# Optimization experiments

Measured on AMD Instinct MI355X. Metric: run time of the kernel, lower is better.

Reference implementation:

```python
import jax, jax.numpy as jnp
import numpy as np

B, D, H = 8192, 256, 512


def setup_inputs() -> dict:
    key = jax.random.key(0)
    ks = jax.random.split(key, 25)
    inp = {
        "x": jax.random.normal(ks[0], (B, D), jnp.float32),
        "h_t": jax.random.normal(ks[1], (B, H), jnp.float32),
        "h_s": jax.random.normal(ks[2], (B, H), jnp.float32),
        "c_t": jax.random.normal(ks[3], (B, H), jnp.float32),
        "c_s": jax.random.normal(ks[4], (B, H), jnp.float32),
    }
    names = ["Ui", "Wti", "Wsi", "bi", "Us", "Wts", "Wss", "bs",
             "Ut", "Wtt", "Wst", "bt", "Uo", "Wto", "Wso", "bo",
             "Uc", "Wtc", "Wsc", "bc"]
    shapes = {"U": (D, H), "W": (H, H), "b": (H,)}
    scale = 0.02  # keep activations in a sane range
    for i, n in enumerate(names):
        s = shapes["U"] if n[0] == "U" else (shapes["b"] if n[0] == "b" else shapes["W"])
        inp[n] = jax.random.normal(ks[5 + i], s, jnp.float32) * scale
    return inp


def reference(x, h_t, h_s, c_t, c_s,
              Ui, Wti, Wsi, bi, Us, Wts, Wss, bs,
              Ut, Wtt, Wst, bt, Uo, Wto, Wso, bo,
              Uc, Wtc, Wsc, bc):
    # Fuse the 15 small GEMMs into 3 concatenated GEMMs: [B,D]@[D,5H] etc.
    U = jnp.concatenate([Ui, Us, Ut, Uo, Uc], axis=1)      # [D, 5H]
    Wt = jnp.concatenate([Wti, Wts, Wtt, Wto, Wtc], axis=1)  # [H, 5H]
    Ws = jnp.concatenate([Wsi, Wss, Wst, Wso, Wsc], axis=1)  # [H, 5H]
    b = jnp.concatenate([bi, bs, bt, bo, bc])                # [5H]
    gates = x @ U + h_t @ Wt + h_s @ Ws + b                  # [B, 5H]
    g_i, g_fs, g_ft, g_o, g_c = jnp.split(gates, 5, axis=1)
    i_n = jax.nn.sigmoid(g_i)
    f_s_n = jax.nn.sigmoid(g_fs)
    f_t_n = jax.nn.sigmoid(g_ft)
    o_n = jax.nn.sigmoid(g_o)
    c_n = jnp.tanh(g_c)
    c_h = i_n * c_n + f_t_n * c_t + f_s_n * c_s
    h = o_n * jnp.tanh(c_h)
    return (h, c_h)
```

## Files before the change

### kernel.cpp

```cpp
#include <hip/hip_runtime.h>
#include <hip/hip_bf16.h>
#include <cstdint>
#include <cstddef>

#define B_  8192
#define D_  256
#define H_  512
#define K_  1280
#define N_  2560
#define NT_ 320
#define BM_ 256
#define BK_ 64

typedef short short8  __attribute__((ext_vector_type(8)));
typedef float f32x4   __attribute__((ext_vector_type(4)));
typedef float f32x16  __attribute__((ext_vector_type(16)));

__device__ __forceinline__ float sigf(float x)     { return 1.f / (1.f + __expf(-x)); }
__device__ __forceinline__ float tanhfast(float x) { return 1.f - 2.f / (__expf(2.f * x) + 1.f); }

struct WPtrs {
    const float* U[5];
    const float* Wt[5];
    const float* Ws[5];
};

__global__ void prep_a_kernel(const float* __restrict__ x, const float* __restrict__ ht,
                              const float* __restrict__ hs, __hip_bfloat16* __restrict__ A) {
    int t = blockIdx.x * 256 + threadIdx.x;
    int idx8 = t * 8;
    int b = idx8 / K_;
    int k = idx8 - b * K_;
    const float* src;
    if (k < D_)            src = x  + (size_t)b * D_ + k;
    else if (k < D_ + H_)  src = ht + (size_t)b * H_ + (k - D_);
    else                   src = hs + (size_t)b * H_ + (k - D_ - H_);
    f32x4 v0 = *(const f32x4*)(src);
    f32x4 v1 = *(const f32x4*)(src + 4);
    union { short8 s; __hip_bfloat16 h[8]; } o;
    o.h[0] = __float2bfloat16(v0[0]); o.h[1] = __float2bfloat16(v0[1]);
    o.h[2] = __float2bfloat16(v0[2]); o.h[3] = __float2bfloat16(v0[3]);
    o.h[4] = __float2bfloat16(v1[0]); o.h[5] = __float2bfloat16(v1[1]);
    o.h[6] = __float2bfloat16(v1[2]); o.h[7] = __float2bfloat16(v1[3]);
    *(short8*)(A + idx8) = o.s;
}

__global__ void prep_w_kernel(WPtrs p, __hip_bfloat16* __restrict__ WT) {
    __shared__ __hip_bfloat16 tile[64][66];
    int bid2 = blockIdx.x;
    int hblk = bid2 & 7;
    int kblk = (bid2 >> 3) % 20;
    int g    = bid2 / 160;
    int k0 = kblk * 64;
    int h0 = hblk * 64;
    const float* src; int kl0;
    if (k0 < 256)      { src = p.U[g];  kl0 = k0; }
    else if (k0 < 768) { src = p.Wt[g]; kl0 = k0 - 256; }
    else               { src = p.Ws[g]; kl0 = k0 - 768; }
    int tid = threadIdx.x;
    int tk = tid >> 6;
    int th = tid & 63;
    for (int r = 0; r < 16; ++r) {
        int kl = r * 4 + tk;
        tile[kl][th] = __float2bfloat16(src[(size_t)(kl0 + kl) * H_ + h0 + th]);
    }
    __syncthreads();
    for (int r = 0; r < 16; ++r) {
        int hl = r * 4 + tk;
        int h  = h0 + hl;
        int np = (h >> 5) * 160 + g * 32 + (h & 31);
        WT[(size_t)np * K_ + k0 + th] = tile[th][hl];
    }
}

#define GLD16(gp, lp)                                                              \
    __builtin_amdgcn_global_load_lds(                                              \
        (const __attribute__((address_space(1))) unsigned int*)(gp),               \
        (__attribute__((address_space(3))) unsigned int*)(lp), 16, 0, 0)

__global__ __launch_bounds__(512, 2) void gemm_fused_kernel(
    const __hip_bfloat16* __restrict__ A, const __hip_bfloat16* __restrict__ WT,
    const float* __restrict__ ct, const float* __restrict__ cs,
    const float* __restrict__ bi, const float* __restrict__ bfs,
    const float* __restrict__ bft, const float* __restrict__ bo,
    const float* __restrict__ bc, float* __restrict__ out) {
    __shared__ alignas(16) unsigned short sA[2][BM_ * BK_];
    __shared__ alignas(16) unsigned short sB[2][NT_ * BK_];

    int tid = threadIdx.x;
    int n0 = blockIdx.x * NT_;
    int m0 = blockIdx.y * BM_;
    int wid  = tid >> 6, lane = tid & 63;
    int wm   = wid >> 1;
    int wn   = wid & 1;
    int half = lane >> 5, l31 = lane & 31;

    int hg = blockIdx.x * 2 + wn;
    int h  = hg * 32 + l31;
    float Bi = bi[h], Bfs = bfs[h], Bft = bft[h], Bo = bo[h], Bc = bc[h];

    f32x16 acc[2][5];
#pragma unroll
    for (int i = 0; i < 2; ++i)
#pragma unroll
        for (int j = 0; j < 5; ++j)
            acc[i][j] = (f32x16)(0.f);

    int srow = tid >> 3;
    int cSw  = (tid & 7) ^ (srow & 7);
    const __hip_bfloat16* aSrcB = A  + (size_t)(m0 + srow) * K_ + cSw * 8;
    const __hip_bfloat16* bSrcB = WT + (size_t)(n0 + srow) * K_ + cSw * 8;
    int t8 = tid * 8;

#define STAGE(bufsel, koff)                                                      \
    do {                                                                         \
        _Pragma("unroll")                                                        \
        for (int r_ = 0; r_ < 4; ++r_)                                           \
            GLD16(aSrcB + (size_t)r_ * 64 * K_ + (koff), sA[bufsel] + r_ * 4096 + t8); \
        _Pragma("unroll")                                                        \
        for (int r_ = 0; r_ < 5; ++r_)                                           \
            GLD16(bSrcB + (size_t)r_ * 64 * K_ + (koff), sB[bufsel] + r_ * 4096 + t8); \
    } while (0)

    int arow64[2], brow64[5];
#pragma unroll
    for (int i = 0; i < 2; ++i) arow64[i] = (wm * 64 + i * 32 + l31) * 64;
#pragma unroll
    for (int j = 0; j < 5; ++j) brow64[j] = (wn * 160 + j * 32 + l31) * 64;
    int xr = l31 & 7;
    int pk[4];
#pragma unroll
    for (int ks = 0; ks < 4; ++ks) pk[ks] = ((ks * 2 + half) ^ xr) * 8;

    STAGE(0, 0);
    __syncthreads();

    const int nt = K_ / BK_;
#pragma unroll 2
    for (int t = 0; t < nt; ++t) {
        int cur = t & 1;
        if (t + 1 < nt) STAGE(cur ^ 1, (t + 1) * BK_);
        const unsigned short* sAc = sA[cur];
        const unsigned short* sBc = sB[cur];
#pragma unroll
        for (int ks = 0; ks < 4; ++ks) {
            short8 a[2], b[5];
            int po = pk[ks];
#pragma unroll
            for (int i = 0; i < 2; ++i)
                a[i] = *(const short8*)(sAc + arow64[i] + po);
#pragma unroll
            for (int j = 0; j < 5; ++j)
                b[j] = *(const short8*)(sBc + brow64[j] + po);
            __builtin_amdgcn_s_setprio(1);
#pragma unroll
            for (int j = 0; j < 5; ++j)
#pragma unroll
                for (int i = 0; i < 2; ++i)
                    acc[i][j] = __builtin_amdgcn_mfma_f32_32x32x16_bf16(a[i], b[j], acc[i][j], 0, 0, 0);
            __builtin_amdgcn_s_setprio(0);
        }
        __syncthreads();
    }
#undef STAGE

#pragma unroll
    for (int i = 0; i < 2; ++i) {
        int rbase = m0 + wm * 64 + i * 32 + 4 * half;
#pragma unroll
        for (int r = 0; r < 16; ++r) {
            int row = rbase + (r & 3) + 8 * (r >> 2);
            size_t idx = (size_t)row * H_ + h;
            float i_n  = sigf(acc[i][0][r] + Bi);
            float fs_n = sigf(acc[i][1][r] + Bfs);
            float ft_n = sigf(acc[i][2][r] + Bft);
            float o_n  = sigf(acc[i][3][r] + Bo);
            float c_n  = tanhfast(acc[i][4][r] + Bc);
            float ch   = i_n * c_n + ft_n * ct[idx] + fs_n * cs[idx];
            out[idx] = o_n * tanhfast(ch);
            out[(size_t)B_ * H_ + idx] = ch;
        }
    }
}

struct AllW {
    const float* U[5];
    const float* Wt[5];
    const float* Ws[5];
    const float* bias[5];
};

__global__ __launch_bounds__(512) void fallback_kernel(const float* __restrict__ x,
                                                       const float* __restrict__ ht,
                                                       const float* __restrict__ hs,
                                                       const float* __restrict__ ct,
                                                       const float* __restrict__ cs,
                                                       AllW w, float* __restrict__ out) {
    __shared__ float arow[K_];
    int b = blockIdx.x;
    int h = threadIdx.x;
    for (int k = h; k < K_; k += 512) {
        float v;
        if (k < D_)           v = x[b * D_ + k];
        else if (k < D_ + H_) v = ht[b * H_ + k - D_];
        else                  v = hs[b * H_ + k - D_ - H_];
        arow[k] = v;
    }
    __syncthreads();
    float g[5];
    for (int gi = 0; gi < 5; ++gi) {
        float s = w.bias[gi][h];
        const float* U = w.U[gi];
        for (int k = 0; k < D_; ++k) s += arow[k] * U[(size_t)k * H_ + h];
        const float* Wt = w.Wt[gi];
        for (int k = 0; k < H_; ++k) s += arow[D_ + k] * Wt[(size_t)k * H_ + h];
        const float* Ws = w.Ws[gi];
        for (int k = 0; k < H_; ++k) s += arow[D_ + H_ + k] * Ws[(size_t)k * H_ + h];
        g[gi] = s;
    }
    int idx = b * H_ + h;
    float i_n = sigf(g[0]), fs_n = sigf(g[1]), ft_n = sigf(g[2]), o_n = sigf(g[3]);
    float c_n = tanhfast(g[4]);
    float ch  = i_n * c_n + ft_n * ct[idx] + fs_n * cs[idx];
    out[idx] = o_n * tanhfast(ch);
    out[(size_t)B_ * H_ + idx] = ch;
}

extern "C" void kernel_launch(void* const* d_in, const int* in_sizes, int n_in,
                              void* d_out, int out_size, void* d_ws, size_t ws_size,
                              hipStream_t stream) {
    const float* x  = (const float*)d_in[0];
    const float* ht = (const float*)d_in[1];
    const float* hs = (const float*)d_in[2];
    const float* ct = (const float*)d_in[3];
    const float* cs = (const float*)d_in[4];

    WPtrs wp;
    AllW  aw;
    const float* bias[5];
    for (int g = 0; g < 5; ++g) {
        wp.U[g]  = (const float*)d_in[5 + g * 4 + 0];
        wp.Wt[g] = (const float*)d_in[5 + g * 4 + 1];
        wp.Ws[g] = (const float*)d_in[5 + g * 4 + 2];
        bias[g]  = (const float*)d_in[5 + g * 4 + 3];
        aw.U[g] = wp.U[g]; aw.Wt[g] = wp.Wt[g]; aw.Ws[g] = wp.Ws[g]; aw.bias[g] = bias[g];
    }
    float* out = (float*)d_out;

    size_t szA = (size_t)B_ * K_ * 2;
    size_t szW = (size_t)N_ * K_ * 2;

    if (ws_size >= szA + szW) {
        __hip_bfloat16* Abf = (__hip_bfloat16*)d_ws;
        __hip_bfloat16* WT  = (__hip_bfloat16*)((char*)d_ws + szA);

        prep_a_kernel<<<5120, 256, 0, stream>>>(x, ht, hs, Abf);
        prep_w_kernel<<<800, 256, 0, stream>>>(wp, WT);
        gemm_fused_kernel<<<dim3(N_ / NT_, B_ / BM_), 512, 0, stream>>>(
            Abf, WT, ct, cs, bias[0], bias[1], bias[2], bias[3], bias[4], out);
    } else {
        fallback_kernel<<<B_, 512, 0, stream>>>(x, ht, hs, ct, cs, aw, out);
    }
}
```

Before: 234.5 us.

## Halve GEMM block to 256 threads with 4x5 MFMA tiles per wave

The fused GEMM now runs 256 threads (4 waves) per block instead of 512. Each wave computes a 128x160 output tile (4x5 MFMA 32x32 accumulators) instead of 64x160, which raises register-level reuse of the B fragments. The grid is transposed so blockIdx.x walks M, and the LDS swizzle is changed to a 4-way XOR on (row>>1). The price is 320 accumulator registers per lane and single-block occupancy, which could cause spills or poor latency hiding. Global-to-LDS staging now issues twice as many loads per thread.

```diff
diff --git a/kernel.cpp b/kernel.cpp
--- a/kernel.cpp
+++ b/kernel.cpp
@@ -78,7 +78,7 @@
         (const __attribute__((address_space(1))) unsigned int*)(gp),               \
         (__attribute__((address_space(3))) unsigned int*)(lp), 16, 0, 0)
 
-__global__ __launch_bounds__(512, 2) void gemm_fused_kernel(
+__global__ __launch_bounds__(256, 1) void gemm_fused_kernel(
     const __hip_bfloat16* __restrict__ A, const __hip_bfloat16* __restrict__ WT,
     const float* __restrict__ ct, const float* __restrict__ cs,
     const float* __restrict__ bi, const float* __restrict__ bfs,
@@ -88,75 +88,76 @@
     __shared__ alignas(16) unsigned short sB[2][NT_ * BK_];
 
     int tid = threadIdx.x;
-    int n0 = blockIdx.x * NT_;
-    int m0 = blockIdx.y * BM_;
+    int m0 = blockIdx.x * BM_;
+    int n0 = blockIdx.y * NT_;
     int wid  = tid >> 6, lane = tid & 63;
     int wm   = wid >> 1;
     int wn   = wid & 1;
     int half = lane >> 5, l31 = lane & 31;
 
-    int hg = blockIdx.x * 2 + wn;
+    int hg = blockIdx.y * 2 + wn;
     int h  = hg * 32 + l31;
     float Bi = bi[h], Bfs = bfs[h], Bft = bft[h], Bo = bo[h], Bc = bc[h];
 
-    f32x16 acc[2][5];
-#pragma unroll
-    for (int i = 0; i < 2; ++i)
+    f32x16 acc[4][5];
+#pragma unroll
+    for (int i = 0; i < 4; ++i)
 #pragma unroll
         for (int j = 0; j < 5; ++j)
             acc[i][j] = (f32x16)(0.f);
 
-    int srow = tid >> 3;
-    int cSw  = (tid & 7) ^ (srow & 7);
-    const __hip_bfloat16* aSrcB = A  + (size_t)(m0 + srow) * K_ + cSw * 8;
-    const __hip_bfloat16* bSrcB = WT + (size_t)(n0 + srow) * K_ + cSw * 8;
+    int r0  = tid >> 3;
+    int kcS = ((tid & 7) ^ ((r0 >> 1) & 3)) * 8;
+    const __hip_bfloat16* aBase = A  + (size_t)(m0 + r0) * K_ + kcS;
+    const __hip_bfloat16* bBase = WT + (size_t)(n0 + r0) * K_ + kcS;
     int t8 = tid * 8;
 
-#define STAGE(bufsel, koff)                                                      \
-    do {                                                                         \
-        _Pragma("unroll")                                                        \
-        for (int r_ = 0; r_ < 4; ++r_)                                           \
-            GLD16(aSrcB + (size_t)r_ * 64 * K_ + (koff), sA[bufsel] + r_ * 4096 + t8); \
-        _Pragma("unroll")                                                        \
-        for (int r_ = 0; r_ < 5; ++r_)                                           \
-            GLD16(bSrcB + (size_t)r_ * 64 * K_ + (koff), sB[bufsel] + r_ * 4096 + t8); \
+#define STAGE(bufsel, koff)                                                       \
+    do {                                                                          \
+        _Pragma("unroll")                                                         \
+        for (int i_ = 0; i_ < 8; ++i_)                                            \
+            GLD16(aBase + (size_t)i_ * 32 * K_ + (koff), sA[bufsel] + i_ * 2048 + t8); \
+        _Pragma("unroll")                                                         \
+        for (int i_ = 0; i_ < 10; ++i_)                                           \
+            GLD16(bBase + (size_t)i_ * 32 * K_ + (koff), sB[bufsel] + i_ * 2048 + t8); \
     } while (0)
 
-    int arow64[2], brow64[5];
-#pragma unroll
-    for (int i = 0; i < 2; ++i) arow64[i] = (wm * 64 + i * 32 + l31) * 64;
-#pragma unroll
-    for (int j = 0; j < 5; ++j) brow64[j] = (wn * 160 + j * 32 + l31) * 64;
-    int xr = l31 & 7;
-    int pk[4];
-#pragma unroll
-    for (int ks = 0; ks < 4; ++ks) pk[ks] = ((ks * 2 + half) ^ xr) * 8;
+    int arow[4], brow[5], aswz[4], bswz[5];
+#pragma unroll
+    for (int i = 0; i < 4; ++i) {
+        arow[i] = (wm * 128 + i * 32 + l31);
+        aswz[i] = (arow[i] >> 1) & 3;
+    }
+#pragma unroll
+    for (int j = 0; j < 5; ++j) {
+        brow[j] = (wn * 160 + j * 32 + l31);
+        bswz[j] = (brow[j] >> 1) & 3;
+    }
 
     STAGE(0, 0);
     __syncthreads();
 
     const int nt = K_ / BK_;
-#pragma unroll 2
     for (int t = 0; t < nt; ++t) {
         int cur = t & 1;
-        if (t + 1 < nt) STAGE(cur ^ 1, (t + 1) * BK_);
+        if (t + 1 < nt) STAGE(cur ^ 1, (size_t)(t + 1) * BK_);
         const unsigned short* sAc = sA[cur];
         const unsigned short* sBc = sB[cur];
 #pragma unroll
         for (int ks = 0; ks < 4; ++ks) {
-            short8 a[2], b[5];
-            int po = pk[ks];
-#pragma unroll
-            for (int i = 0; i < 2; ++i)
-                a[i] = *(const short8*)(sAc + arow64[i] + po);
+            short8 a[4], b[5];
+            int g = ks * 2 + half;
+#pragma unroll
+            for (int i = 0; i < 4; ++i)
+                a[i] = *(const short8*)(sAc + arow[i] * 64 + (g ^ aswz[i]) * 8);
 #pragma unroll
             for (int j = 0; j < 5; ++j)
-                b[j] = *(const short8*)(sBc + brow64[j] + po);
+                b[j] = *(const short8*)(sBc + brow[j] * 64 + (g ^ bswz[j]) * 8);
             __builtin_amdgcn_s_setprio(1);
 #pragma unroll
             for (int j = 0; j < 5; ++j)
 #pragma unroll
-                for (int i = 0; i < 2; ++i)
+                for (int i = 0; i < 4; ++i)
                     acc[i][j] = __builtin_amdgcn_mfma_f32_32x32x16_bf16(a[i], b[j], acc[i][j], 0, 0, 0);
             __builtin_amdgcn_s_setprio(0);
         }
@@ -165,8 +166,8 @@
 #undef STAGE
 
 #pragma unroll
-    for (int i = 0; i < 2; ++i) {
-        int rbase = m0 + wm * 64 + i * 32 + 4 * half;
+    for (int i = 0; i < 4; ++i) {
+        int rbase = m0 + wm * 128 + i * 32 + 4 * half;
 #pragma unroll
         for (int r = 0; r < 16; ++r) {
             int row = rbase + (r & 3) + 8 * (r >> 2);
@@ -256,7 +257,7 @@
 
         prep_a_kernel<<<5120, 256, 0, stream>>>(x, ht, hs, Abf);
         prep_w_kernel<<<800, 256, 0, stream>>>(wp, WT);
-        gemm_fused_kernel<<<dim3(N_ / NT_, B_ / BM_), 512, 0, stream>>>(
+        gemm_fused_kernel<<<dim3(B_ / BM_, N_ / NT_), 256, 0, stream>>>(
             Abf, WT, ct, cs, bias[0], bias[1], bias[2], bias[3], bias[4], out);
     } else {
         fallback_kernel<<<B_, 512, 0, stream>>>(x, ht, hs, ct, cs, aw, out);
```

Result: slower. 339.9 us (+44.9%).

## Interleave global-to-LDS prefetch across k-substeps with explicit barriers and waitcnts

Applied to the files above, without the earlier changes.

Restructures the main GEMM loop so the next tile's global-to-LDS loads are split across the four k-substeps (A first, then B in two chunks) instead of issued all at once. Each substep reads its LDS fragments, then uses explicit s_barrier and lgkmcnt/vmcnt waits before and after the MFMAs, similar to a ping-pong schedule. The aim is to spread memory traffic and overlap it better with MFMA work. The cost is eight barriers per k-tile instead of one, which may add synchronisation stalls.

```diff
diff --git a/kernel.cpp b/kernel.cpp
--- a/kernel.cpp
+++ b/kernel.cpp
@@ -94,6 +94,7 @@
     int wm   = wid >> 1;
     int wn   = wid & 1;
     int half = lane >> 5, l31 = lane & 31;
+    int xr   = l31 & 7;
 
     int hg = blockIdx.x * 2 + wn;
     int h  = hg * 32 + l31;
@@ -107,62 +108,106 @@
             acc[i][j] = (f32x16)(0.f);
 
     int srow = tid >> 3;
-    int cSw  = (tid & 7) ^ (srow & 7);
-    const __hip_bfloat16* aSrcB = A  + (size_t)(m0 + srow) * K_ + cSw * 8;
-    const __hip_bfloat16* bSrcB = WT + (size_t)(n0 + srow) * K_ + cSw * 8;
+    int kcS  = ((tid & 7) ^ (srow & 7)) * 8;
+    const __hip_bfloat16* aBase = A  + (size_t)(m0 + srow) * K_ + kcS;
+    const __hip_bfloat16* bBase = WT + (size_t)(n0 + srow) * K_ + kcS;
     int t8 = tid * 8;
 
-#define STAGE(bufsel, koff)                                                      \
-    do {                                                                         \
-        _Pragma("unroll")                                                        \
-        for (int r_ = 0; r_ < 4; ++r_)                                           \
-            GLD16(aSrcB + (size_t)r_ * 64 * K_ + (koff), sA[bufsel] + r_ * 4096 + t8); \
-        _Pragma("unroll")                                                        \
-        for (int r_ = 0; r_ < 5; ++r_)                                           \
-            GLD16(bSrcB + (size_t)r_ * 64 * K_ + (koff), sB[bufsel] + r_ * 4096 + t8); \
+#define STG_A(dst, koff)                                                        \
+    do {                                                                        \
+        _Pragma("unroll")                                                       \
+        for (int r_ = 0; r_ < 4; ++r_)                                          \
+            GLD16(aBase + (size_t)r_ * 64 * K_ + (koff), (dst) + r_ * 4096 + t8); \
     } while (0)
+#define STG_B(dst, koff, rlo, rhi)                                              \
+    do {                                                                        \
+        _Pragma("unroll")                                                       \
+        for (int r_ = (rlo); r_ < (rhi); ++r_)                                  \
+            GLD16(bBase + (size_t)r_ * 64 * K_ + (koff), (dst) + r_ * 4096 + t8); \
+    } while (0)
 
     int arow64[2], brow64[5];
 #pragma unroll
     for (int i = 0; i < 2; ++i) arow64[i] = (wm * 64 + i * 32 + l31) * 64;
 #pragma unroll
     for (int j = 0; j < 5; ++j) brow64[j] = (wn * 160 + j * 32 + l31) * 64;
-    int xr = l31 & 7;
-    int pk[4];
-#pragma unroll
-    for (int ks = 0; ks < 4; ++ks) pk[ks] = ((ks * 2 + half) ^ xr) * 8;
-
-    STAGE(0, 0);
-    __syncthreads();
+
+#define READS(ks_)                                                              \
+    int po_ = (((ks_) * 2 + half) ^ xr) * 8;                                    \
+    short8 a0 = *(const short8*)(sAc + arow64[0] + po_);                        \
+    short8 a1 = *(const short8*)(sAc + arow64[1] + po_);                        \
+    short8 b0 = *(const short8*)(sBc + brow64[0] + po_);                        \
+    short8 b1 = *(const short8*)(sBc + brow64[1] + po_);                        \
+    short8 b2 = *(const short8*)(sBc + brow64[2] + po_);                        \
+    short8 b3 = *(const short8*)(sBc + brow64[3] + po_);                        \
+    short8 b4 = *(const short8*)(sBc + brow64[4] + po_)
+
+#define MFMAS()                                                                 \
+    __builtin_amdgcn_s_setprio(1);                                              \
+    acc[0][0] = __builtin_amdgcn_mfma_f32_32x32x16_bf16(a0, b0, acc[0][0], 0, 0, 0); \
+    acc[1][0] = __builtin_amdgcn_mfma_f32_32x32x16_bf16(a1, b0, acc[1][0], 0, 0, 0); \
+    acc[0][1] = __builtin_amdgcn_mfma_f32_32x32x16_bf16(a0, b1, acc[0][1], 0, 0, 0); \
+    acc[1][1] = __builtin_amdgcn_mfma_f32_32x32x16_bf16(a1, b1, acc[1][1], 0, 0, 0); \
+    acc[0][2] = __builtin_amdgcn_mfma_f32_32x32x16_bf16(a0, b2, acc[0][2], 0, 0, 0); \
+    acc[1][2] = __builtin_amdgcn_mfma_f32_32x32x16_bf16(a1, b2, acc[1][2], 0, 0, 0); \
+    acc[0][3] = __builtin_amdgcn_mfma_f32_32x32x16_bf16(a0, b3, acc[0][3], 0, 0, 0); \
+    acc[1][3] = __builtin_amdgcn_mfma_f32_32x32x16_bf16(a1, b3, acc[1][3], 0, 0, 0); \
+    acc[0][4] = __builtin_amdgcn_mfma_f32_32x32x16_bf16(a0, b4, acc[0][4], 0, 0, 0); \
+    acc[1][4] = __builtin_amdgcn_mfma_f32_32x32x16_bf16(a1, b4, acc[1][4], 0, 0, 0); \
+    __builtin_amdgcn_s_setprio(0)
+
+#define BAR()   __builtin_amdgcn_s_barrier()
+#define LGKM0() asm volatile("s_waitcnt lgkmcnt(0)" ::: "memory")
+#define VM0()   asm volatile("s_waitcnt vmcnt(0)" ::: "memory")
+
+    STG_A(sA[0], 0);
+    STG_B(sB[0], 0, 0, 5);
+    VM0();
+    BAR();
 
     const int nt = K_ / BK_;
 #pragma unroll 2
     for (int t = 0; t < nt; ++t) {
-        int cur = t & 1;
-        if (t + 1 < nt) STAGE(cur ^ 1, (t + 1) * BK_);
-        const unsigned short* sAc = sA[cur];
-        const unsigned short* sBc = sB[cur];
-#pragma unroll
-        for (int ks = 0; ks < 4; ++ks) {
-            short8 a[2], b[5];
-            int po = pk[ks];
-#pragma unroll
-            for (int i = 0; i < 2; ++i)
-                a[i] = *(const short8*)(sAc + arow64[i] + po);
-#pragma unroll
-            for (int j = 0; j < 5; ++j)
-                b[j] = *(const short8*)(sBc + brow64[j] + po);
-            __builtin_amdgcn_s_setprio(1);
-#pragma unroll
-            for (int j = 0; j < 5; ++j)
-#pragma unroll
-                for (int i = 0; i < 2; ++i)
-                    acc[i][j] = __builtin_amdgcn_mfma_f32_32x32x16_bf16(a[i], b[j], acc[i][j], 0, 0, 0);
-            __builtin_amdgcn_s_setprio(0);
-        }
-        __syncthreads();
-    }
-#undef STAGE
+        const unsigned short* sAc = sA[t & 1];
+        const unsigned short* sBc = sB[t & 1];
+        unsigned short* sAn = sA[(t & 1) ^ 1];
+        unsigned short* sBn = sB[(t & 1) ^ 1];
+        const bool pf = (t + 1 < nt);
+        const int ko = (t + 1) * BK_;
+
+        {
+            if (pf) STG_A(sAn, ko);
+            READS(0);
+            BAR(); LGKM0();
+            MFMAS();
+            BAR();
+        }
+        {
+            if (pf) STG_B(sBn, ko, 0, 3);
+            READS(1);
+            BAR(); LGKM0();
+            MFMAS();
+            BAR();
+        }
+        {
+            if (pf) STG_B(sBn, ko, 3, 5);
+            READS(2);
+            BAR(); LGKM0();
+            MFMAS();
+            BAR();
+        }
+        {
+            READS(3);
+            BAR(); LGKM0();
+            MFMAS();
+            VM0();
+            BAR();
+        }
+    }
+#undef STG_A
+#undef STG_B
+#undef READS
+#undef MFMAS
 
 #pragma unroll
     for (int i = 0; i < 2; ++i) {
```

Result: slower. 241.3 us (+2.9%).

## Fuse fp32-to-bf16 activation conversion into GEMM A-tile loading

Applied to the files above, without the earlier changes.

Drops the separate prep kernel that turned x, h_t and h_s into a bf16 concatenated A matrix. The GEMM now loads fp32 activations straight into registers, converts them and writes the swizzled bf16 tile into LDS, interleaved with the MFMA k-steps. This removes one kernel launch and the write and re-read of the bf16 A buffer. In exchange each GEMM block reads fp32 A (twice the bytes) once per N-tile column (8 column blocks), and the A loads become synchronous register loads instead of async global-to-LDS copies, which may add latency and register pressure.

```diff
diff --git a/kernel.cpp b/kernel.cpp
--- a/kernel.cpp
+++ b/kernel.cpp
@@ -24,26 +24,6 @@
     const float* Wt[5];
     const float* Ws[5];
 };
-
-__global__ void prep_a_kernel(const float* __restrict__ x, const float* __restrict__ ht,
-                              const float* __restrict__ hs, __hip_bfloat16* __restrict__ A) {
-    int t = blockIdx.x * 256 + threadIdx.x;
-    int idx8 = t * 8;
-    int b = idx8 / K_;
-    int k = idx8 - b * K_;
-    const float* src;
-    if (k < D_)            src = x  + (size_t)b * D_ + k;
-    else if (k < D_ + H_)  src = ht + (size_t)b * H_ + (k - D_);
-    else                   src = hs + (size_t)b * H_ + (k - D_ - H_);
-    f32x4 v0 = *(const f32x4*)(src);
-    f32x4 v1 = *(const f32x4*)(src + 4);
-    union { short8 s; __hip_bfloat16 h[8]; } o;
-    o.h[0] = __float2bfloat16(v0[0]); o.h[1] = __float2bfloat16(v0[1]);
-    o.h[2] = __float2bfloat16(v0[2]); o.h[3] = __float2bfloat16(v0[3]);
-    o.h[4] = __float2bfloat16(v1[0]); o.h[5] = __float2bfloat16(v1[1]);
-    o.h[6] = __float2bfloat16(v1[2]); o.h[7] = __float2bfloat16(v1[3]);
-    *(short8*)(A + idx8) = o.s;
-}
 
 __global__ void prep_w_kernel(WPtrs p, __hip_bfloat16* __restrict__ WT) {
     __shared__ __hip_bfloat16 tile[64][66];
@@ -79,7 +59,8 @@
         (__attribute__((address_space(3))) unsigned int*)(lp), 16, 0, 0)
 
 __global__ __launch_bounds__(512, 2) void gemm_fused_kernel(
-    const __hip_bfloat16* __restrict__ A, const __hip_bfloat16* __restrict__ WT,
+    const float* __restrict__ x, const float* __restrict__ ht,
+    const float* __restrict__ hs, const __hip_bfloat16* __restrict__ WT,
     const float* __restrict__ ct, const float* __restrict__ cs,
     const float* __restrict__ bi, const float* __restrict__ bfs,
     const float* __restrict__ bft, const float* __restrict__ bo,
@@ -94,6 +75,7 @@
     int wm   = wid >> 1;
     int wn   = wid & 1;
     int half = lane >> 5, l31 = lane & 31;
+    int xr   = l31 & 7;
 
     int hg = blockIdx.x * 2 + wn;
     int h  = hg * 32 + l31;
@@ -107,19 +89,54 @@
             acc[i][j] = (f32x16)(0.f);
 
     int srow = tid >> 3;
-    int cSw  = (tid & 7) ^ (srow & 7);
-    const __hip_bfloat16* aSrcB = A  + (size_t)(m0 + srow) * K_ + cSw * 8;
-    const __hip_bfloat16* bSrcB = WT + (size_t)(n0 + srow) * K_ + cSw * 8;
+    int pA   = tid & 7;
+    int xk   = srow & 7;
+
+    const __hip_bfloat16* bBase = WT + (size_t)(n0 + srow) * K_ + (pA ^ xk) * 8;
     int t8 = tid * 8;
-
-#define STAGE(bufsel, koff)                                                      \
-    do {                                                                         \
-        _Pragma("unroll")                                                        \
-        for (int r_ = 0; r_ < 4; ++r_)                                           \
-            GLD16(aSrcB + (size_t)r_ * 64 * K_ + (koff), sA[bufsel] + r_ * 4096 + t8); \
-        _Pragma("unroll")                                                        \
-        for (int r_ = 0; r_ < 5; ++r_)                                           \
-            GLD16(bSrcB + (size_t)r_ * 64 * K_ + (koff), sB[bufsel] + r_ * 4096 + t8); \
+#define STG_B(dst, koff)                                                          \
+    do {                                                                          \
+        _Pragma("unroll")                                                         \
+        for (int r_ = 0; r_ < 5; ++r_)                                            \
+            GLD16(bBase + (size_t)r_ * 64 * K_ + (koff), (dst) + r_ * 4096 + t8); \
+    } while (0)
+
+    int rowIdx = m0 + srow;
+    const float* xB  = x  + (size_t)rowIdx * D_ + pA * 8;
+    const float* htB = ht + (size_t)rowIdx * H_ + pA * 8;
+    const float* hsB = hs + (size_t)rowIdx * H_ + pA * 8;
+    int aWr = srow * 64 + (pA ^ xk) * 8;
+
+#define A_SRC(k0n, aP, aStr)                                                      \
+    do {                                                                          \
+        if ((k0n) < 256)      { aP = xB + (k0n);        aStr = 64 * D_; }         \
+        else if ((k0n) < 768) { aP = htB + ((k0n)-256); aStr = 64 * H_; }         \
+        else                  { aP = hsB + ((k0n)-768); aStr = 64 * H_; }         \
+    } while (0)
+
+#define A_LOAD2(av, aP, aStr, r0_)                                                \
+    do {                                                                          \
+        av[0][0] = *(const f32x4*)((aP) + (size_t)((r0_)) * (aStr));              \
+        av[0][1] = *(const f32x4*)((aP) + (size_t)((r0_)) * (aStr) + 4);          \
+        av[1][0] = *(const f32x4*)((aP) + (size_t)((r0_) + 1) * (aStr));          \
+        av[1][1] = *(const f32x4*)((aP) + (size_t)((r0_) + 1) * (aStr) + 4);      \
+    } while (0)
+
+#define A_CVTWR(dst, av, r0_)                                                     \
+    do {                                                                          \
+        _Pragma("unroll")                                                         \
+        for (int q_ = 0; q_ < 2; ++q_) {                                          \
+            union { short8 s; __hip_bfloat16 hh[8]; } o_;                         \
+            o_.hh[0] = __float2bfloat16(av[q_][0][0]);                            \
+            o_.hh[1] = __float2bfloat16(av[q_][0][1]);                            \
+            o_.hh[2] = __float2bfloat16(av[q_][0][2]);                            \
+            o_.hh[3] = __float2bfloat16(av[q_][0][3]);                            \
+            o_.hh[4] = __float2bfloat16(av[q_][1][0]);                            \
+            o_.hh[5] = __float2bfloat16(av[q_][1][1]);                            \
+            o_.hh[6] = __float2bfloat16(av[q_][1][2]);                            \
+            o_.hh[7] = __float2bfloat16(av[q_][1][3]);                            \
+            *(short8*)((dst) + ((r0_) + q_) * 4096 + aWr) = o_.s;                 \
+        }                                                                         \
     } while (0)
 
     int arow64[2], brow64[5];
@@ -127,42 +144,74 @@
     for (int i = 0; i < 2; ++i) arow64[i] = (wm * 64 + i * 32 + l31) * 64;
 #pragma unroll
     for (int j = 0; j < 5; ++j) brow64[j] = (wn * 160 + j * 32 + l31) * 64;
-    int xr = l31 & 7;
-    int pk[4];
-#pragma unroll
-    for (int ks = 0; ks < 4; ++ks) pk[ks] = ((ks * 2 + half) ^ xr) * 8;
-
-    STAGE(0, 0);
+
+#define KSTEP(ks_)                                                                     \
+    do {                                                                               \
+        int po_ = (((ks_) * 2 + half) ^ xr) * 8;                                       \
+        short8 a0 = *(const short8*)(sAc + arow64[0] + po_);                           \
+        short8 a1 = *(const short8*)(sAc + arow64[1] + po_);                           \
+        short8 b0 = *(const short8*)(sBc + brow64[0] + po_);                           \
+        short8 b1 = *(const short8*)(sBc + brow64[1] + po_);                           \
+        short8 b2 = *(const short8*)(sBc + brow64[2] + po_);                           \
+        short8 b3 = *(const short8*)(sBc + brow64[3] + po_);                           \
+        short8 b4 = *(const short8*)(sBc + brow64[4] + po_);                           \
+        __builtin_amdgcn_s_setprio(1);                                                 \
+        acc[0][0] = __builtin_amdgcn_mfma_f32_32x32x16_bf16(a0, b0, acc[0][0], 0, 0, 0); \
+        acc[1][0] = __builtin_amdgcn_mfma_f32_32x32x16_bf16(a1, b0, acc[1][0], 0, 0, 0); \
+        acc[0][1] = __builtin_amdgcn_mfma_f32_32x32x16_bf16(a0, b1, acc[0][1], 0, 0, 0); \
+        acc[1][1] = __builtin_amdgcn_mfma_f32_32x32x16_bf16(a1, b1, acc[1][1], 0, 0, 0); \
+        acc[0][2] = __builtin_amdgcn_mfma_f32_32x32x16_bf16(a0, b2, acc[0][2], 0, 0, 0); \
+        acc[1][2] = __builtin_amdgcn_mfma_f32_32x32x16_bf16(a1, b2, acc[1][2], 0, 0, 0); \
+        acc[0][3] = __builtin_amdgcn_mfma_f32_32x32x16_bf16(a0, b3, acc[0][3], 0, 0, 0); \
+        acc[1][3] = __builtin_amdgcn_mfma_f32_32x32x16_bf16(a1, b3, acc[1][3], 0, 0, 0); \
+        acc[0][4] = __builtin_amdgcn_mfma_f32_32x32x16_bf16(a0, b4, acc[0][4], 0, 0, 0); \
+        acc[1][4] = __builtin_amdgcn_mfma_f32_32x32x16_bf16(a1, b4, acc[1][4], 0, 0, 0); \
+        __builtin_amdgcn_s_setprio(0);                                                 \
+    } while (0)
+
+    {
+        STG_B(sB[0], 0);
+        const float* aP; int aStr;
+        A_SRC(0, aP, aStr);
+        f32x4 av[2][2];
+        A_LOAD2(av, aP, aStr, 0); A_CVTWR(sA[0], av, 0);
+        A_LOAD2(av, aP, aStr, 2); A_CVTWR(sA[0], av, 2);
+    }
     __syncthreads();
 
     const int nt = K_ / BK_;
-#pragma unroll 2
     for (int t = 0; t < nt; ++t) {
-        int cur = t & 1;
-        if (t + 1 < nt) STAGE(cur ^ 1, (t + 1) * BK_);
+        const int cur = t & 1;
         const unsigned short* sAc = sA[cur];
         const unsigned short* sBc = sB[cur];
-#pragma unroll
-        for (int ks = 0; ks < 4; ++ks) {
-            short8 a[2], b[5];
-            int po = pk[ks];
-#pragma unroll
-            for (int i = 0; i < 2; ++i)
-                a[i] = *(const short8*)(sAc + arow64[i] + po);
-#pragma unroll
-            for (int j = 0; j < 5; ++j)
-                b[j] = *(const short8*)(sBc + brow64[j] + po);
-            __builtin_amdgcn_s_setprio(1);
-#pragma unroll
-            for (int j = 0; j < 5; ++j)
-#pragma unroll
-                for (int i = 0; i < 2; ++i)
-                    acc[i][j] = __builtin_amdgcn_mfma_f32_32x32x16_bf16(a[i], b[j], acc[i][j], 0, 0, 0);
-            __builtin_amdgcn_s_setprio(0);
+        unsigned short* sAn = sA[cur ^ 1];
+        unsigned short* sBn = sB[cur ^ 1];
+        const bool pf = (t + 1 < nt);
+        const int kon = (t + 1) * BK_;
+
+        const float* aP = nullptr; int aStr = 0;
+        f32x4 av[2][2];
+        if (pf) {
+            A_SRC(kon, aP, aStr);
+            STG_B(sBn, kon);
+            A_LOAD2(av, aP, aStr, 0);
         }
+        KSTEP(0);
+        KSTEP(1);
+        if (pf) {
+            A_CVTWR(sAn, av, 0);
+            A_LOAD2(av, aP, aStr, 2);
+        }
+        KSTEP(2);
+        KSTEP(3);
+        if (pf) A_CVTWR(sAn, av, 2);
         __syncthreads();
     }
-#undef STAGE
+#undef KSTEP
+#undef STG_B
+#undef A_SRC
+#undef A_LOAD2
+#undef A_CVTWR
 
 #pragma unroll
     for (int i = 0; i < 2; ++i) {
@@ -247,17 +296,14 @@
     }
     float* out = (float*)d_out;
 
-    size_t szA = (size_t)B_ * K_ * 2;
     size_t szW = (size_t)N_ * K_ * 2;
 
-    if (ws_size >= szA + szW) {
-        __hip_bfloat16* Abf = (__hip_bfloat16*)d_ws;
-        __hip_bfloat16* WT  = (__hip_bfloat16*)((char*)d_ws + szA);
-
-        prep_a_kernel<<<5120, 256, 0, stream>>>(x, ht, hs, Abf);
+    if (ws_size >= szW) {
+        __hip_bfloat16* WT = (__hip_bfloat16*)d_ws;
+
         prep_w_kernel<<<800, 256, 0, stream>>>(wp, WT);
         gemm_fused_kernel<<<dim3(N_ / NT_, B_ / BM_), 512, 0, stream>>>(
-            Abf, WT, ct, cs, bias[0], bias[1], bias[2], bias[3], bias[4], out);
+            x, ht, hs, WT, ct, cs, bias[0], bias[1], bias[2], bias[3], bias[4], out);
     } else {
         fallback_kernel<<<B_, 512, 0, stream>>>(x, ht, hs, ct, cs, aw, out);
     }
```

New measurement: 233.1 us. No clear change (-0.6%).
